# Kernel tuning notes

Hardware: AMD Instinct MI355X
Metric: run time of the kernel (lower is better)

Reference implementation:

```python
import jax, jax.numpy as jnp
import numpy as np

EPS = 1e-16
S = 20  # amino-acid alphabet size, hardcoded in original (reshape to (-1,20,20))


def make_rate_matrix(R, p):
    """R: (n,S,S) symmetric, zero diag; p: (n,S) equilibrium. Returns normalized Q: (n,S,S)."""
    Q = R * p[:, None, :]
    diag = jnp.sum(Q, axis=-1, keepdims=True)          # (n,S,1)
    Q = Q - diag * jnp.eye(S, dtype=p.dtype)           # put -rowsum on diagonal
    mue = jnp.sum(p[..., None] * diag, axis=-2, keepdims=True)  # (n,1,1) expected mutation rate
    return Q / jnp.maximum(mue, EPS)


def setup_inputs() -> dict:
    key = jax.random.key(0)
    k1, k2, k3, k4, k5 = jax.random.split(key, 5)
    m, b, L, k, num_rates = 2, 512, 512, 2, 512
    sequences = jax.random.randint(k1, (m, b, L), 0, S, dtype=jnp.int32)
    rate_indices = jax.random.randint(k2, (m, b), 0, num_rates, dtype=jnp.int32)
    tau_kernel = jax.random.normal(k3, (m, num_rates), dtype=jnp.float32) - 3.0  # rate_init = const(-3)
    exchangeability_kernel = jax.random.normal(k4, (m, k, S, S), dtype=jnp.float32)
    equilibrium_kernel = jax.random.normal(k5, (m, k, S), dtype=jnp.float32)
    return {"sequences": sequences, "rate_indices": rate_indices, "tau_kernel": tau_kernel,
            "exchangeability_kernel": exchangeability_kernel, "equilibrium_kernel": equilibrium_kernel}


def reference(sequences, rate_indices, tau_kernel, exchangeability_kernel, equilibrium_kernel):
    m, k = exchangeability_kernel.shape[:2]
    b = sequences.shape[1]
    # make_R: symmetrize, softplus, zero diagonal
    R = jax.nn.softplus(0.5 * (exchangeability_kernel + jnp.swapaxes(exchangeability_kernel, -1, -2)))
    R = R * (1.0 - jnp.eye(S, dtype=R.dtype))
    # make_p: softmax equilibrium
    p = jax.nn.softmax(equilibrium_kernel, axis=-1)
    # normalized rate matrices Q: (m,k,S,S)
    Q = make_rate_matrix(R.reshape(-1, S, S), p.reshape(-1, S)).reshape(m, k, S, S)
    # make_tau: gather per-sequence time, softplus
    tau = jax.nn.softplus(tau_kernel[jnp.arange(m)[:, None], rate_indices])  # (m,b)
    # tau*Q and batched matrix exponential: (m,b,k,S,S)
    tauQ = tau[:, :, None, None, None] * Q[:, None]
    P = jax.scipy.linalg.expm(tauQ)
    # embedding-lookup combine: ancprobs[m,b,l,k,:] = P[m,b,k,seq[m,b,l],:]
    P_t = jnp.transpose(P, (0, 1, 3, 2, 4))  # (m,b,S,k,S)
    mi = jnp.arange(m)[:, None, None]
    bi = jnp.arange(b)[None, :, None]
    ancprobs = P_t[mi, bi, sequences]  # (m,b,L,k,S)
    return ancprobs
```

## Files before the change

kernel.cpp:

```cpp
#include <hip/hip_runtime.h>
#include <math.h>

#define SA 20
#define KDIM 2
#define MDIM 2
#define BDIM 512
#define LDIM 512
#define NRATES 512
#define PPB 4
#define THREADS 256
#define NCH (LDIM * KDIM * SA / 4)

__device__ __forceinline__ float softplusf(float x) {
    return fmaxf(x, 0.0f) + log1pf(expf(-fabsf(x)));
}

__device__ __forceinline__ void mmB(float* C, const float* A, const float* Bl) {
    #pragma unroll
    for (int j = 0; j < SA; ++j) C[j] = 0.0f;
    #pragma unroll
    for (int t = 0; t < SA; ++t) {
        const float a = A[t];
        const float4* row = reinterpret_cast<const float4*>(Bl + t * SA);
        #pragma unroll
        for (int q = 0; q < 5; ++q) {
            float4 b = row[q];
            C[4*q+0] = fmaf(a, b.x, C[4*q+0]);
            C[4*q+1] = fmaf(a, b.y, C[4*q+1]);
            C[4*q+2] = fmaf(a, b.z, C[4*q+2]);
            C[4*q+3] = fmaf(a, b.w, C[4*q+3]);
        }
    }
}

__device__ __forceinline__ void stageRow(float* dst, const float* T, int row, bool act) {
    if (act) {
        float4* d4 = reinterpret_cast<float4*>(dst + row * SA);
        #pragma unroll
        for (int q = 0; q < 5; ++q)
            d4[q] = make_float4(T[4*q+0], T[4*q+1], T[4*q+2], T[4*q+3]);
    }
}

__global__ __launch_bounds__(THREADS) void ancprobs_fused_kernel(
    const int*   __restrict__ seqg,
    const int*   __restrict__ rateIdx,
    const float* __restrict__ tauk,
    const float* __restrict__ Ek,
    const float* __restrict__ eqk,
    float*       __restrict__ out)
{
    __shared__ float sP[PPB * KDIM * SA * SA];
    __shared__ int   sSeq[PPB * LDIM];

    const int tid  = threadIdx.x;
    const int w    = tid >> 6;
    const int lane = tid & 63;
    const int mb   = blockIdx.x * PPB + w;
    const int mm   = mb >> 9;

    {
        const int4* sq = reinterpret_cast<const int4*>(seqg + (size_t)mb * LDIM);
        int4* dst = reinterpret_cast<int4*>(sSeq + w * LDIM);
        dst[lane]      = sq[lane];
        dst[lane + 64] = sq[lane + 64];
    }

    const int  half = lane >> 5;
    const int  row  = lane & 31;
    const bool act  = row < SA;
    const int  mk   = mm * KDIM + half;
    float* stage = sP + (w * KDIM + half) * SA * SA;

    float e = act ? eqk[mk * SA + row] : -INFINITY;
    float mx = e;
    #pragma unroll
    for (int off = 16; off; off >>= 1) mx = fmaxf(mx, __shfl_xor(mx, off, 32));
    float ex = act ? expf(e - mx) : 0.0f;
    float sm = ex;
    #pragma unroll
    for (int off = 16; off; off >>= 1) sm += __shfl_xor(sm, off, 32);
    float p_i = ex / sm;

    const int r0 = act ? row : 0;
    float A[SA];
    float dg = 0.0f;
    #pragma unroll
    for (int j = 0; j < SA; ++j) {
        float pj = __shfl(p_i, j, 32);
        float e1 = Ek[(mk * SA + r0) * SA + j];
        float e2 = Ek[(mk * SA + j) * SA + r0];
        float r  = (j == row) ? 0.0f : softplusf(0.5f * (e1 + e2));
        float q  = r * pj;
        A[j] = q;
        dg  += q;
    }
    float t_ = act ? p_i * dg : 0.0f;
    #pragma unroll
    for (int off = 16; off; off >>= 1) t_ += __shfl_xor(t_, off, 32);
    const float inv = 1.0f / fmaxf(t_, 1e-16f);

    const float tau = softplusf(tauk[mm * NRATES + rateIdx[mb]]);
    const float sc  = tau * inv;
    #pragma unroll
    for (int j = 0; j < SA; ++j)
        A[j] = act ? ((j == row) ? -dg * sc : A[j] * sc) : 0.0f;

    float rn = 0.0f;
    #pragma unroll
    for (int j = 0; j < SA; ++j) rn += fabsf(A[j]);
    #pragma unroll
    for (int off = 16; off; off >>= 1) rn = fmaxf(rn, __shfl_xor(rn, off, 32));
    int s = 0;
    if (rn > 1.0f) s = (int)ceilf(log2f(rn));
    if (s < 0) s = 0;
    if (s > 30) s = 30;
    const float scale = exp2f((float)(-s));
    #pragma unroll
    for (int j = 0; j < SA; ++j) A[j] *= scale;
    const int smax = max(s, __shfl_xor(s, 32, 64));

    float A2[SA], A3[SA], T[SA];
    stageRow(stage, A, row, act);
    mmB(A2, A, stage);
    mmB(A3, A2, stage);
    #pragma unroll
    for (int j = 0; j < SA; ++j) {
        float id = (j == row) ? 1.0f : 0.0f;
        T[j] = (1.0f/6.0f)*id + (1.0f/24.0f)*A[j] + (1.0f/120.0f)*A2[j] + (1.0f/720.0f)*A3[j];
    }
    stageRow(stage, T, row, act);
    {
        float P1[SA];
        mmB(P1, A3, stage);
        #pragma unroll
        for (int j = 0; j < SA; ++j) {
            float id = (j == row) ? 1.0f : 0.0f;
            T[j] = P1[j] + id + A[j] + 0.5f * A2[j];
        }
    }
    for (int it = 0; it < smax; ++it) {
        stageRow(stage, T, row, act);
        float Tn[SA];
        mmB(Tn, T, stage);
        const bool doit = it < s;
        #pragma unroll
        for (int j = 0; j < SA; ++j) T[j] = doit ? Tn[j] : T[j];
    }
    stageRow(stage, T, row, act);

    __syncthreads();

    const float4* pv = reinterpret_cast<const float4*>(sP);
    #pragma unroll 1
    for (int pr = 0; pr < PPB; ++pr) {
        float4* o4 = reinterpret_cast<float4*>(out) + (size_t)(blockIdx.x * PPB + pr) * NCH;
        const int* sq = sSeq + pr * LDIM;
        for (int f = tid; f < NCH; f += THREADS) {
            int l  = f / 10;
            int ch = f - l * 10;
            int kk = (ch >= 5) ? 1 : 0;
            int c4 = ch - kk * 5;
            o4[f] = pv[((pr * KDIM + kk) * SA + sq[l]) * 5 + c4];
        }
    }
}

extern "C" void kernel_launch(void* const* d_in, const int* in_sizes, int n_in,
                              void* d_out, int out_size, void* d_ws, size_t ws_size,
                              hipStream_t stream) {
    const int*   seq  = (const int*)d_in[0];
    const int*   ridx = (const int*)d_in[1];
    const float* tauk = (const float*)d_in[2];
    const float* Ek   = (const float*)d_in[3];
    const float* eqk  = (const float*)d_in[4];
    float* out = (float*)d_out;

    ancprobs_fused_kernel<<<(MDIM * BDIM) / PPB, THREADS, 0, stream>>>(
        seq, ridx, tauk, Ek, eqk, out);
}
```

Baseline: 109.7 us.

## Split fused kernel into P-compute and wide gather kernels via workspace

Splits the fused kernel in two. The first kernel computes the per-sequence matrix exponentials into a global workspace. The second is a gather kernel that launches 2048 blocks, each writing half a sequence's output from shared memory, and uses a multiply-shift instead of division for the index. The aim is to spread the large output write across more blocks and raise occupancy, rather than having 256 blocks serialize compute then store. The cost is an extra launch and a round trip of P through global memory, and the old fused path stays as a fallback when the workspace is too small.

Result: slower. 114.3 us (+4.2%).

```diff
diff --git a/kernel.cpp b/kernel.cpp
--- a/kernel.cpp
+++ b/kernel.cpp
@@ -10,6 +10,12 @@
 #define PPB 4
 #define THREADS 256
 #define NCH (LDIM * KDIM * SA / 4)
+#define PFLOATS (KDIM * SA * SA)
+#define WS_NEEDED ((size_t)MDIM * BDIM * PFLOATS * sizeof(float))
+
+#define G_BLOCKS (MDIM * BDIM * 2)
+#define HALF_L (LDIM / 2)
+#define CH_PER_BLOCK (NCH / 2)
 
 __device__ __forceinline__ float softplusf(float x) {
     return fmaxf(x, 0.0f) + log1pf(expf(-fabsf(x)));
@@ -39,6 +45,145 @@
         #pragma unroll
         for (int q = 0; q < 5; ++q)
             d4[q] = make_float4(T[4*q+0], T[4*q+1], T[4*q+2], T[4*q+3]);
+    }
+}
+
+__global__ __launch_bounds__(THREADS) void compute_P_kernel(
+    const int*   __restrict__ rateIdx,
+    const float* __restrict__ tauk,
+    const float* __restrict__ Ek,
+    const float* __restrict__ eqk,
+    float*       __restrict__ Pws)
+{
+    __shared__ float sP[PPB * KDIM * SA * SA];
+
+    const int tid  = threadIdx.x;
+    const int w    = tid >> 6;
+    const int lane = tid & 63;
+    const int mb   = blockIdx.x * PPB + w;
+    const int mm   = mb >> 9;
+
+    const int  half = lane >> 5;
+    const int  row  = lane & 31;
+    const bool act  = row < SA;
+    const int  mk   = mm * KDIM + half;
+    float* stage = sP + (w * KDIM + half) * SA * SA;
+
+    float e = act ? eqk[mk * SA + row] : -INFINITY;
+    float mx = e;
+    #pragma unroll
+    for (int off = 16; off; off >>= 1) mx = fmaxf(mx, __shfl_xor(mx, off, 32));
+    float ex = act ? expf(e - mx) : 0.0f;
+    float sm = ex;
+    #pragma unroll
+    for (int off = 16; off; off >>= 1) sm += __shfl_xor(sm, off, 32);
+    float p_i = ex / sm;
+
+    const int r0 = act ? row : 0;
+    float A[SA];
+    float dg = 0.0f;
+    #pragma unroll
+    for (int j = 0; j < SA; ++j) {
+        float pj = __shfl(p_i, j, 32);
+        float e1 = Ek[(mk * SA + r0) * SA + j];
+        float e2 = Ek[(mk * SA + j) * SA + r0];
+        float r  = (j == row) ? 0.0f : softplusf(0.5f * (e1 + e2));
+        float q  = r * pj;
+        A[j] = q;
+        dg  += q;
+    }
+    float t_ = act ? p_i * dg : 0.0f;
+    #pragma unroll
+    for (int off = 16; off; off >>= 1) t_ += __shfl_xor(t_, off, 32);
+    const float inv = 1.0f / fmaxf(t_, 1e-16f);
+
+    const float tau = softplusf(tauk[mm * NRATES + rateIdx[mb]]);
+    const float sc  = tau * inv;
+    #pragma unroll
+    for (int j = 0; j < SA; ++j)
+        A[j] = act ? ((j == row) ? -dg * sc : A[j] * sc) : 0.0f;
+
+    float rn = 0.0f;
+    #pragma unroll
+    for (int j = 0; j < SA; ++j) rn += fabsf(A[j]);
+    #pragma unroll
+    for (int off = 16; off; off >>= 1) rn = fmaxf(rn, __shfl_xor(rn, off, 32));
+    int s = 0;
+    if (rn > 1.0f) s = (int)ceilf(log2f(rn));
+    if (s < 0) s = 0;
+    if (s > 30) s = 30;
+    const float scale = exp2f((float)(-s));
+    #pragma unroll
+    for (int j = 0; j < SA; ++j) A[j] *= scale;
+    const int smax = max(s, __shfl_xor(s, 32, 64));
+
+    float A2[SA], A3[SA], T[SA];
+    stageRow(stage, A, row, act);
+    mmB(A2, A, stage);
+    mmB(A3, A2, stage);
+    #pragma unroll
+    for (int j = 0; j < SA; ++j) {
+        float id = (j == row) ? 1.0f : 0.0f;
+        T[j] = (1.0f/6.0f)*id + (1.0f/24.0f)*A[j] + (1.0f/120.0f)*A2[j] + (1.0f/720.0f)*A3[j];
+    }
+    stageRow(stage, T, row, act);
+    {
+        float P1[SA];
+        mmB(P1, A3, stage);
+        #pragma unroll
+        for (int j = 0; j < SA; ++j) {
+            float id = (j == row) ? 1.0f : 0.0f;
+            T[j] = P1[j] + id + A[j] + 0.5f * A2[j];
+        }
+    }
+    for (int it = 0; it < smax; ++it) {
+        stageRow(stage, T, row, act);
+        float Tn[SA];
+        mmB(Tn, T, stage);
+        const bool doit = it < s;
+        #pragma unroll
+        for (int j = 0; j < SA; ++j) T[j] = doit ? Tn[j] : T[j];
+    }
+
+    if (act) {
+        float4* d4 = reinterpret_cast<float4*>(
+            Pws + ((size_t)(mb * KDIM + half) * SA + row) * SA);
+        #pragma unroll
+        for (int q = 0; q < 5; ++q)
+            d4[q] = make_float4(T[4*q+0], T[4*q+1], T[4*q+2], T[4*q+3]);
+    }
+}
+
+__global__ __launch_bounds__(256, 8) void gather_out_kernel(
+    const int*   __restrict__ seqg,
+    const float* __restrict__ Pws,
+    float*       __restrict__ out)
+{
+    __shared__ float4 sP4[PFLOATS / 4];
+    __shared__ int    sSeq[HALF_L];
+
+    const int tid  = threadIdx.x;
+    const int bid  = blockIdx.x;
+    const int mb   = bid >> 1;
+    const int half = bid & 1;
+
+    if (tid < PFLOATS / 4)
+        sP4[tid] = reinterpret_cast<const float4*>(Pws)[mb * (PFLOATS / 4) + tid];
+    sSeq[tid] = seqg[mb * LDIM + half * HALF_L + tid];
+    __syncthreads();
+
+    float4* o4 = reinterpret_cast<float4*>(out)
+               + (size_t)mb * NCH + (size_t)half * CH_PER_BLOCK;
+
+    #pragma unroll
+    for (int i = 0; i < CH_PER_BLOCK / 256; ++i) {
+        const int lf = tid + i * 256;
+        const int l  = (lf * 6554) >> 16;
+        const int ch = lf - l * 10;
+        const int kk = (ch >= 5) ? 1 : 0;
+        const int c4 = ch - kk * 5;
+        const int sq = sSeq[l];
+        o4[lf] = sP4[(kk * SA + sq) * 5 + c4];
     }
 }
 
@@ -176,6 +321,13 @@
     const float* eqk  = (const float*)d_in[4];
     float* out = (float*)d_out;
 
-    ancprobs_fused_kernel<<<(MDIM * BDIM) / PPB, THREADS, 0, stream>>>(
-        seq, ridx, tauk, Ek, eqk, out);
-}
+    if (d_ws != nullptr && ws_size >= WS_NEEDED) {
+        float* Pws = (float*)d_ws;
+        compute_P_kernel<<<(MDIM * BDIM) / PPB, THREADS, 0, stream>>>(
+            ridx, tauk, Ek, eqk, Pws);
+        gather_out_kernel<<<G_BLOCKS, 256, 0, stream>>>(seq, Pws, out);
+    } else {
+        ancprobs_fused_kernel<<<(MDIM * BDIM) / PPB, THREADS, 0, stream>>>(
+            seq, ridx, tauk, Ek, eqk, out);
+    }
+}
```
